# Performance work log

Hardware: AMD Instinct MI355X
Metric: run time of the kernel (lower is better)

Reference implementation:

```python
import jax, jax.numpy as jnp
import numpy as np

B, S, D = 8, 1024, 1024
H, DH = 16, 64  # n_heads, d_head; D == H*DH


def setup_inputs() -> dict:
    key = jax.random.key(0)
    ks = jax.random.split(key, 7)
    scale = 1.0 / np.sqrt(DH)
    return {
        "images": jax.random.normal(ks[0], (B, S, D), dtype=jnp.float32),
        "Wq": jax.random.normal(ks[1], (H, DH, DH), dtype=jnp.float32) * scale,
        "bq": jax.random.normal(ks[2], (H, DH), dtype=jnp.float32) * scale,
        "Wk": jax.random.normal(ks[3], (H, DH, DH), dtype=jnp.float32) * scale,
        "bk": jax.random.normal(ks[4], (H, DH), dtype=jnp.float32) * scale,
        "Wv": jax.random.normal(ks[5], (H, DH, DH), dtype=jnp.float32) * scale,
        "bv": jax.random.normal(ks[6], (H, DH), dtype=jnp.float32) * scale,
    }


def reference(images, Wq, bq, Wk, bk, Wv, bv):
    Bn, Sn, Dn = images.shape
    x = images.reshape(Bn, Sn, H, DH)  # split hidden dim into per-head slices
    # torch Linear: y = x @ W.T + b, per head -> einsum over input dim d
    q = jnp.einsum("bshd,hod->bsho", x, Wq) + bq  # [B,S,H,DH]
    k = jnp.einsum("bshd,hod->bsho", x, Wk) + bk
    v = jnp.einsum("bshd,hod->bsho", x, Wv) + bv
    scores = jnp.einsum("bqhd,bkhd->bhqk", q, k) / jnp.sqrt(jnp.asarray(DH, x.dtype))
    attn = jax.nn.softmax(scores, axis=-1)  # [B,H,S,S]
    out = jnp.einsum("bhqk,bkhd->bqhd", attn, v)  # [B,S,H,DH]
    return out.reshape(Bn, Sn, Dn)  # hstack across heads == reshape back
```

## Files before the change

### kernel.cpp

```cpp
#include <hip/hip_runtime.h>
#include <hip/hip_bf16.h>

#define B_ 8
#define S_ 1024
#define D_ 1024
#define H_ 16
#define DH_ 64

typedef __attribute__((ext_vector_type(8))) short short8;
typedef __attribute__((ext_vector_type(8))) unsigned short ushort8;
typedef __attribute__((ext_vector_type(4))) unsigned short us4;
typedef __attribute__((ext_vector_type(4))) unsigned int uint4v;
typedef __attribute__((ext_vector_type(4))) float f32x4;

#define QSCALE 0.18033688011112042f

static __device__ __forceinline__ unsigned short f2bf(float f) {
    union { float f; unsigned u; } v; v.f = f;
    unsigned r = v.u + 0x7fffu + ((v.u >> 16) & 1u);
    return (unsigned short)(r >> 16);
}

static __device__ __forceinline__ void stage8(const float* __restrict__ src, unsigned short* dst) {
    float4 a = *reinterpret_cast<const float4*>(src);
    float4 b = *reinterpret_cast<const float4*>(src + 4);
    ushort8 r;
    r[0] = f2bf(a.x); r[1] = f2bf(a.y); r[2] = f2bf(a.z); r[3] = f2bf(a.w);
    r[4] = f2bf(b.x); r[5] = f2bf(b.y); r[6] = f2bf(b.z); r[7] = f2bf(b.w);
    *reinterpret_cast<ushort8*>(dst) = r;
}

static __device__ __forceinline__ unsigned int cvtpk(float a, float b) {
    unsigned int r;
    asm("v_cvt_pk_bf16_f32 %0, %1, %2" : "=v"(r) : "v"(a), "v"(b));
    return r;
}

static __device__ __forceinline__ void gll16(const void* g, void* l) {
    __builtin_amdgcn_global_load_lds(
        (const __attribute__((address_space(1))) unsigned int*)g,
        (__attribute__((address_space(3))) unsigned int*)l,
        16, 0, 0);
}

__global__ __launch_bounds__(256) void qkv_proj(
    const float* __restrict__ x,
    const float* __restrict__ Wq, const float* __restrict__ bq,
    const float* __restrict__ Wk, const float* __restrict__ bk,
    const float* __restrict__ Wv, const float* __restrict__ bv,
    unsigned short* __restrict__ qo, unsigned short* __restrict__ ko,
    unsigned short* __restrict__ vo)
{
    const int bid   = blockIdx.x;
    const int stile = bid & 15;
    const int h     = (bid >> 4) & (H_ - 1);
    const int b     = bid >> 8;
    const int tid   = threadIdx.x;
    const int lane  = tid & 63;
    const int wave  = tid >> 6;
    const int lr    = lane & 15;
    const int lk    = lane >> 4;

    __shared__ __align__(16) unsigned short xs[64][72];
    __shared__ __align__(16) unsigned short wsh[3][64][72];

    {
        int row = tid >> 2;
        int col = (tid & 3) * 16;
        const float* src = x + ((size_t)(b * S_ + stile * 64 + row)) * D_ + h * DH_ + col;
        stage8(src,     &xs[row][col]);
        stage8(src + 8, &xs[row][col + 8]);
        const float* wsrc[3] = { Wq + h * DH_ * DH_, Wk + h * DH_ * DH_, Wv + h * DH_ * DH_ };
        #pragma unroll
        for (int p = 0; p < 3; ++p) {
            const float* s = wsrc[p] + row * DH_ + col;
            stage8(s,     &wsh[p][row][col]);
            stage8(s + 8, &wsh[p][row][col + 8]);
        }
    }
    __syncthreads();

    short8 a[2];
    #pragma unroll
    for (int kk = 0; kk < 2; ++kk)
        a[kk] = *reinterpret_cast<const short8*>(&xs[wave * 16 + lr][8 * lk + 32 * kk]);

    f32x4 acc[3][4];
    #pragma unroll
    for (int p = 0; p < 3; ++p)
        #pragma unroll
        for (int n = 0; n < 4; ++n)
            acc[p][n] = (f32x4){0.f, 0.f, 0.f, 0.f};

    #pragma unroll
    for (int p = 0; p < 3; ++p)
        #pragma unroll
        for (int kk = 0; kk < 2; ++kk)
            #pragma unroll
            for (int n = 0; n < 4; ++n) {
                short8 bf = *reinterpret_cast<const short8*>(&wsh[p][lr + 16 * n][8 * lk + 32 * kk]);
                acc[p][n] = __builtin_amdgcn_mfma_f32_16x16x32_bf16(a[kk], bf, acc[p][n], 0, 0, 0);
            }

    size_t base = ((size_t)(b * H_ + h) * S_ + stile * 64 + wave * 16) * DH_;
    #pragma unroll
    for (int p = 0; p < 2; ++p) {
        const float* bias = p ? (bk + h * DH_) : (bq + h * DH_);
        unsigned short* op = p ? ko : qo;
        #pragma unroll
        for (int n = 0; n < 4; ++n) {
            int col = lr + 16 * n;
            float bb = bias[col];
            #pragma unroll
            for (int r = 0; r < 4; ++r) {
                float val = acc[p][n][r] + bb;
                if (p == 0) val *= QSCALE;
                op[base + (size_t)(4 * lk + r) * DH_ + col] = f2bf(val);
            }
        }
    }
    {
        size_t vbase = (size_t)(b * H_ + h) * DH_ * S_;
        int s0 = stile * 64 + wave * 16 + 4 * lk;
        #pragma unroll
        for (int n = 0; n < 4; ++n) {
            int dh = lr + 16 * n;
            float bb = bv[h * DH_ + dh];
            us4 w;
            #pragma unroll
            for (int r = 0; r < 4; ++r) w[r] = f2bf(acc[2][n][r] + bb);
            *reinterpret_cast<us4*>(vo + vbase + (size_t)dh * S_ + s0) = w;
        }
    }
}

__global__ __launch_bounds__(256, 4) void attn_fwd(
    const unsigned short* __restrict__ q,
    const unsigned short* __restrict__ k,
    const unsigned short* __restrict__ vt,
    float* __restrict__ out)
{
    const int bid   = (blockIdx.x & 7) * 128 + (blockIdx.x >> 3);
    const int qtile = bid & 7;
    const int h     = (bid >> 3) & (H_ - 1);
    const int b     = bid >> 7;
    const int tid   = threadIdx.x;
    const int lane  = tid & 63;
    const int wave  = tid >> 6;
    const int lr    = lane & 15;
    const int lk    = lane >> 4;

    __shared__ __align__(16) unsigned short ks[2][64][64];
    __shared__ __align__(16) unsigned short vs[2][64][64];

    const size_t bh = (size_t)(b * H_ + h) * S_ * DH_;

    short8 qf[2][2];
    #pragma unroll
    for (int g = 0; g < 2; ++g) {
        const unsigned short* qp = q + bh + (size_t)(qtile * 128 + wave * 32 + 16 * g + lr) * DH_;
        #pragma unroll
        for (int kk = 0; kk < 2; ++kk)
            qf[g][kk] = *reinterpret_cast<const short8*>(qp + 8 * lk + 32 * kk);
    }

    const int rp0 = 16 * wave + (lane >> 3);
    const int rp1 = rp0 + 8;
    const int c   = lane & 7;
    const int gk0 = (rp0 & 0x23) | ((rp0 & 0x10) >> 2) | ((rp0 & 0x0C) << 1);
    const int gk1 = (rp1 & 0x23) | ((rp1 & 0x10) >> 2) | ((rp1 & 0x0C) << 1);
    const size_t kofs0 = (size_t)gk0 * DH_ + (c ^ (rp0 & 7)) * 8;
    const size_t kofs1 = (size_t)gk1 * DH_ + (c ^ (rp1 & 7)) * 8;
    const size_t vofs0 = (size_t)rp0 * S_ + (c ^ (rp0 & 7)) * 8;
    const size_t vofs1 = (size_t)rp1 * S_ + (c ^ (rp1 & 7)) * 8;
    const unsigned short* kb = k + bh;
    const unsigned short* vb = vt + bh;

    gll16(kb + kofs0, &ks[0][16 * wave][0]);
    gll16(kb + kofs1, &ks[0][16 * wave + 8][0]);
    gll16(vb + vofs0, &vs[0][16 * wave][0]);
    gll16(vb + vofs1, &vs[0][16 * wave + 8][0]);

    f32x4 acc[2][4];
    #pragma unroll
    for (int g = 0; g < 2; ++g)
        #pragma unroll
        for (int n = 0; n < 4; ++n) acc[g][n] = (f32x4){0.f, 0.f, 0.f, 0.f};
    float l0 = 0.f, l1 = 0.f;

    const int rx = lr & 7;
    const int NT = S_ / 64;
    for (int t = 0; t < NT; ++t) {
        __syncthreads();
        const int cur = t & 1;

        if (t + 1 < NT) {
            const int nxt = cur ^ 1;
            const unsigned short* kt  = kb + (size_t)(t + 1) * 64 * DH_;
            const unsigned short* vtb = vb + (size_t)(t + 1) * 64;
            gll16(kt + kofs0,  &ks[nxt][16 * wave][0]);
            gll16(kt + kofs1,  &ks[nxt][16 * wave + 8][0]);
            gll16(vtb + vofs0, &vs[nxt][16 * wave][0]);
            gll16(vtb + vofs1, &vs[nxt][16 * wave + 8][0]);
        }

        f32x4 st[2][4];
        #pragma unroll
        for (int g = 0; g < 2; ++g)
            #pragma unroll
            for (int n = 0; n < 4; ++n) st[g][n] = (f32x4){0.f, 0.f, 0.f, 0.f};
        #pragma unroll
        for (int kk = 0; kk < 2; ++kk)
            #pragma unroll
            for (int n = 0; n < 4; ++n) {
                short8 ka = *reinterpret_cast<const short8*>(
                    &ks[cur][16 * n + lr][((lk + 4 * kk) ^ rx) * 8]);
                st[0][n] = __builtin_amdgcn_mfma_f32_16x16x32_bf16(ka, qf[0][kk], st[0][n], 0, 0, 0);
                st[1][n] = __builtin_amdgcn_mfma_f32_16x16x32_bf16(ka, qf[1][kk], st[1][n], 0, 0, 0);
            }

        #pragma unroll
        for (int g = 0; g < 2; ++g)
            #pragma unroll
            for (int n = 0; n < 4; ++n)
                #pragma unroll
                for (int r = 0; r < 4; ++r)
                    st[g][n][r] = __builtin_amdgcn_exp2f(st[g][n][r]);
        {
            float a0 = (st[0][0][0] + st[0][0][1]) + (st[0][0][2] + st[0][0][3]);
            float a1 = (st[0][1][0] + st[0][1][1]) + (st[0][1][2] + st[0][1][3]);
            float a2 = (st[0][2][0] + st[0][2][1]) + (st[0][2][2] + st[0][2][3]);
            float a3 = (st[0][3][0] + st[0][3][1]) + (st[0][3][2] + st[0][3][3]);
            l0 += (a0 + a1) + (a2 + a3);
            float b0 = (st[1][0][0] + st[1][0][1]) + (st[1][0][2] + st[1][0][3]);
            float b1 = (st[1][1][0] + st[1][1][1]) + (st[1][1][2] + st[1][1][3]);
            float b2 = (st[1][2][0] + st[1][2][1]) + (st[1][2][2] + st[1][2][3]);
            float b3 = (st[1][3][0] + st[1][3][1]) + (st[1][3][2] + st[1][3][3]);
            l1 += (b0 + b1) + (b2 + b3);
        }

        short8 pa[2][2];
        #pragma unroll
        for (int g = 0; g < 2; ++g)
            #pragma unroll
            for (int kk = 0; kk < 2; ++kk) {
                uint4v w4;
                w4[0] = cvtpk(st[g][2 * kk][0],     st[g][2 * kk][1]);
                w4[1] = cvtpk(st[g][2 * kk][2],     st[g][2 * kk][3]);
                w4[2] = cvtpk(st[g][2 * kk + 1][0], st[g][2 * kk + 1][1]);
                w4[3] = cvtpk(st[g][2 * kk + 1][2], st[g][2 * kk + 1][3]);
                pa[g][kk] = __builtin_bit_cast(short8, w4);
            }

        #pragma unroll
        for (int kk = 0; kk < 2; ++kk)
            #pragma unroll
            for (int n = 0; n < 4; ++n) {
                short8 va = *reinterpret_cast<const short8*>(
                    &vs[cur][16 * n + lr][((lk + 4 * kk) ^ rx) * 8]);
                acc[0][n] = __builtin_amdgcn_mfma_f32_16x16x32_bf16(va, pa[0][kk], acc[0][n], 0, 0, 0);
                acc[1][n] = __builtin_amdgcn_mfma_f32_16x16x32_bf16(va, pa[1][kk], acc[1][n], 0, 0, 0);
            }
    }

    l0 += __shfl_xor(l0, 16, 64); l0 += __shfl_xor(l0, 32, 64);
    l1 += __shfl_xor(l1, 16, 64); l1 += __shfl_xor(l1, 32, 64);
    const float inv0 = 1.f / l0, inv1 = 1.f / l1;
    #pragma unroll
    for (int g = 0; g < 2; ++g) {
        const float inv = g ? inv1 : inv0;
        const int qrow = qtile * 128 + wave * 32 + 16 * g + lr;
        float* op = out + (size_t)(b * S_ + qrow) * D_ + h * DH_;
        #pragma unroll
        for (int n = 0; n < 4; ++n) {
            float4 o;
            o.x = acc[g][n][0] * inv; o.y = acc[g][n][1] * inv;
            o.z = acc[g][n][2] * inv; o.w = acc[g][n][3] * inv;
            *reinterpret_cast<float4*>(op + 16 * n + 4 * lk) = o;
        }
    }
}

extern "C" void kernel_launch(void* const* d_in, const int* in_sizes, int n_in,
                              void* d_out, int out_size, void* d_ws, size_t ws_size,
                              hipStream_t stream) {
    const float* x  = (const float*)d_in[0];
    const float* Wq = (const float*)d_in[1];
    const float* bq = (const float*)d_in[2];
    const float* Wk = (const float*)d_in[3];
    const float* bk = (const float*)d_in[4];
    const float* Wv = (const float*)d_in[5];
    const float* bv = (const float*)d_in[6];
    float* out = (float*)d_out;

    unsigned short* qw = (unsigned short*)d_ws;
    size_t per = (size_t)B_ * H_ * S_ * DH_;
    unsigned short* kw = qw + per;
    unsigned short* vw = kw + per;

    qkv_proj<<<dim3(B_ * H_ * (S_ / 64)), 256, 0, stream>>>(x, Wq, bq, Wk, bk, Wv, bv, qw, kw, vw);
    attn_fwd<<<dim3(B_ * H_ * (S_ / 128)), 256, 0, stream>>>(qw, kw, vw, out);
}
```

Before: 68.47 us.

## Compute softmax row sums with MFMA against ones and store Q transposed

The per-tile VALU reduction of exponentiated scores is replaced by extra MFMA instructions that multiply a vector of bf16 ones by the packed P fragments. The row sum now comes from the bf16-rounded probabilities, which makes it consistent with the PV product. The projection kernel now writes Q transposed, like V, using vectorized 4-element stores instead of scalar stores. The attention kernel then gathers Q fragments with strided scalar loads, but it does this only once per block. The aim is to remove VALU adds from the inner loop and cheapen the Q store, at the cost of 4 extra MFMAs per tile.

Result: no change. 68.51 us (+0.1%).

```diff
diff --git a/kernel.cpp b/kernel.cpp
--- a/kernel.cpp
+++ b/kernel.cpp
@@ -102,34 +102,34 @@
                 acc[p][n] = __builtin_amdgcn_mfma_f32_16x16x32_bf16(a[kk], bf, acc[p][n], 0, 0, 0);
             }
 
-    size_t base = ((size_t)(b * H_ + h) * S_ + stile * 64 + wave * 16) * DH_;
-    #pragma unroll
-    for (int p = 0; p < 2; ++p) {
-        const float* bias = p ? (bk + h * DH_) : (bq + h * DH_);
-        unsigned short* op = p ? ko : qo;
+    {
+        size_t base = ((size_t)(b * H_ + h) * S_ + stile * 64 + wave * 16) * DH_;
+        const float* bias = bk + h * DH_;
         #pragma unroll
         for (int n = 0; n < 4; ++n) {
             int col = lr + 16 * n;
             float bb = bias[col];
             #pragma unroll
-            for (int r = 0; r < 4; ++r) {
-                float val = acc[p][n][r] + bb;
-                if (p == 0) val *= QSCALE;
-                op[base + (size_t)(4 * lk + r) * DH_ + col] = f2bf(val);
-            }
-        }
-    }
-    {
-        size_t vbase = (size_t)(b * H_ + h) * DH_ * S_;
+            for (int r = 0; r < 4; ++r)
+                ko[base + (size_t)(4 * lk + r) * DH_ + col] = f2bf(acc[1][n][r] + bb);
+        }
+    }
+    {
+        size_t tbase = (size_t)(b * H_ + h) * DH_ * S_;
         int s0 = stile * 64 + wave * 16 + 4 * lk;
         #pragma unroll
         for (int n = 0; n < 4; ++n) {
             int dh = lr + 16 * n;
-            float bb = bv[h * DH_ + dh];
-            us4 w;
-            #pragma unroll
-            for (int r = 0; r < 4; ++r) w[r] = f2bf(acc[2][n][r] + bb);
-            *reinterpret_cast<us4*>(vo + vbase + (size_t)dh * S_ + s0) = w;
+            float bbq = bq[h * DH_ + dh];
+            float bbv = bv[h * DH_ + dh];
+            us4 wq, wv;
+            #pragma unroll
+            for (int r = 0; r < 4; ++r) {
+                wq[r] = f2bf((acc[0][n][r] + bbq) * QSCALE);
+                wv[r] = f2bf(acc[2][n][r] + bbv);
+            }
+            *reinterpret_cast<us4*>(qo + tbase + (size_t)dh * S_ + s0) = wq;
+            *reinterpret_cast<us4*>(vo + tbase + (size_t)dh * S_ + s0) = wv;
         }
     }
 }
@@ -156,12 +156,27 @@
     const size_t bh = (size_t)(b * H_ + h) * S_ * DH_;
 
     short8 qf[2][2];
-    #pragma unroll
-    for (int g = 0; g < 2; ++g) {
-        const unsigned short* qp = q + bh + (size_t)(qtile * 128 + wave * 32 + 16 * g + lr) * DH_;
-        #pragma unroll
-        for (int kk = 0; kk < 2; ++kk)
-            qf[g][kk] = *reinterpret_cast<const short8*>(qp + 8 * lk + 32 * kk);
+    {
+        const unsigned short* qb = q + bh;
+        const int qrow0 = qtile * 128 + wave * 32 + lr;
+        #pragma unroll
+        for (int g = 0; g < 2; ++g)
+            #pragma unroll
+            for (int kk = 0; kk < 2; ++kk) {
+                ushort8 tmp;
+                #pragma unroll
+                for (int j = 0; j < 8; ++j)
+                    tmp[j] = qb[(size_t)(8 * lk + 32 * kk + j) * S_ + qrow0 + 16 * g];
+                qf[g][kk] = __builtin_bit_cast(short8, tmp);
+            }
+    }
+
+    short8 ones;
+    {
+        ushort8 ou;
+        #pragma unroll
+        for (int j = 0; j < 8; ++j) ou[j] = 0x3F80;
+        ones = __builtin_bit_cast(short8, ou);
     }
 
     const int rp0 = 16 * wave + (lane >> 3);
@@ -181,12 +196,13 @@
     gll16(vb + vofs0, &vs[0][16 * wave][0]);
     gll16(vb + vofs1, &vs[0][16 * wave + 8][0]);
 
-    f32x4 acc[2][4];
-    #pragma unroll
-    for (int g = 0; g < 2; ++g)
+    f32x4 acc[2][4], accl[2];
+    #pragma unroll
+    for (int g = 0; g < 2; ++g) {
         #pragma unroll
         for (int n = 0; n < 4; ++n) acc[g][n] = (f32x4){0.f, 0.f, 0.f, 0.f};
-    float l0 = 0.f, l1 = 0.f;
+        accl[g] = (f32x4){0.f, 0.f, 0.f, 0.f};
+    }
 
     const int rx = lr & 7;
     const int NT = S_ / 64;
@@ -226,18 +242,6 @@
                 #pragma unroll
                 for (int r = 0; r < 4; ++r)
                     st[g][n][r] = __builtin_amdgcn_exp2f(st[g][n][r]);
-        {
-            float a0 = (st[0][0][0] + st[0][0][1]) + (st[0][0][2] + st[0][0][3]);
-            float a1 = (st[0][1][0] + st[0][1][1]) + (st[0][1][2] + st[0][1][3]);
-            float a2 = (st[0][2][0] + st[0][2][1]) + (st[0][2][2] + st[0][2][3]);
-            float a3 = (st[0][3][0] + st[0][3][1]) + (st[0][3][2] + st[0][3][3]);
-            l0 += (a0 + a1) + (a2 + a3);
-            float b0 = (st[1][0][0] + st[1][0][1]) + (st[1][0][2] + st[1][0][3]);
-            float b1 = (st[1][1][0] + st[1][1][1]) + (st[1][1][2] + st[1][1][3]);
-            float b2 = (st[1][2][0] + st[1][2][1]) + (st[1][2][2] + st[1][2][3]);
-            float b3 = (st[1][3][0] + st[1][3][1]) + (st[1][3][2] + st[1][3][3]);
-            l1 += (b0 + b1) + (b2 + b3);
-        }
 
         short8 pa[2][2];
         #pragma unroll
@@ -253,7 +257,7 @@
             }
 
         #pragma unroll
-        for (int kk = 0; kk < 2; ++kk)
+        for (int kk = 0; kk < 2; ++kk) {
             #pragma unroll
             for (int n = 0; n < 4; ++n) {
                 short8 va = *reinterpret_cast<const short8*>(
@@ -261,14 +265,14 @@
                 acc[0][n] = __builtin_amdgcn_mfma_f32_16x16x32_bf16(va, pa[0][kk], acc[0][n], 0, 0, 0);
                 acc[1][n] = __builtin_amdgcn_mfma_f32_16x16x32_bf16(va, pa[1][kk], acc[1][n], 0, 0, 0);
             }
-    }
-
-    l0 += __shfl_xor(l0, 16, 64); l0 += __shfl_xor(l0, 32, 64);
-    l1 += __shfl_xor(l1, 16, 64); l1 += __shfl_xor(l1, 32, 64);
-    const float inv0 = 1.f / l0, inv1 = 1.f / l1;
+            accl[0] = __builtin_amdgcn_mfma_f32_16x16x32_bf16(ones, pa[0][kk], accl[0], 0, 0, 0);
+            accl[1] = __builtin_amdgcn_mfma_f32_16x16x32_bf16(ones, pa[1][kk], accl[1], 0, 0, 0);
+        }
+    }
+
     #pragma unroll
     for (int g = 0; g < 2; ++g) {
-        const float inv = g ? inv1 : inv0;
+        const float inv = 1.f / accl[g][0];
         const int qrow = qtile * 128 + wave * 32 + 16 * g + lr;
         float* op = out + (size_t)(b * S_ + qrow) * D_ + h * DH_;
         #pragma unroll
```
